# Performance work log

Measured on AMD Instinct MI355X. Metric: run time of the kernel, lower is better.

## Reference

```python
import jax, jax.numpy as jnp
import numpy as np


def _build_tree(N: int, n: int, seed: int = 0):
    """Random forest encoded as parent pointers + sibling ranks.

    parents:  int32 [N+1]; parents[i] in [0, i) for i>0, root(0) and sentinel(N) -> N.
    child_pos: int32 [N+1]; rank among siblings (in_edges order); >= n means the
               one-hot code is all zeros (matches torch.eye rows beyond n, and roots).
    """
    rng = np.random.default_rng(seed)
    parents = np.empty(N + 1, dtype=np.int32)
    parents[0] = N                      # root -> sentinel
    parents[1:N] = rng.integers(0, np.arange(1, N))  # parent of i is an earlier node
    parents[N] = N                      # sentinel self-loop

    pa = parents[:N].astype(np.int64)
    order = np.argsort(pa, kind="stable")
    sorted_pa = pa[order]
    _, first_idx, inv = np.unique(sorted_pa, return_index=True, return_inverse=True)
    rank = np.arange(N) - first_idx[inv]           # sibling rank within each parent group
    child_pos = np.empty(N + 1, dtype=np.int32)
    child_pos[order] = rank.astype(np.int32)
    child_pos[0] = n                    # root has no parent -> zero code
    child_pos[N] = n                    # sentinel -> zero code
    return parents, child_pos


def setup_inputs() -> dict:
    N, n, k = 262144, 32, 16
    parents, child_pos = _build_tree(N, n)
    return {
        "parents": jnp.asarray(parents),
        "child_pos": jnp.asarray(child_pos),
        "n": n,
        "k": k,
    }


def reference(parents, child_pos, n, k):
    """pos_embeds[node] = concat_{t=0..k-1} onehot(child_pos(ancestor_t(node)), n).

    This is the closed form of the original layer-by-layer scatter:
      pos[child, :n]  = eye row (sibling rank one-hot)
      pos[child, n:]  = pos[parent, :-n]
    Roots keep all-zero codes (child_pos = n -> out-of-range one-hot = zeros).
    """
    N = parents.shape[0] - 1

    def step(cur, _):
        code = jax.nn.one_hot(child_pos[cur], n, dtype=jnp.float32)  # [N, n]
        return parents[cur], code

    _, codes = jax.lax.scan(step, jnp.arange(N, dtype=parents.dtype), None, length=k)
    # codes: [k, N, n] -> [N, k*n] with slot 0 (own code) first
    return jnp.transpose(codes, (1, 0, 2)).reshape(N, k * n)
```

## Files before the change

kernel.cpp:

```cpp
#include <hip/hip_runtime.h>


#define NN 32
#define KK 16

typedef float f32x4 __attribute__((ext_vector_type(4)));

__global__ __launch_bounds__(256) void pe_fused_rl(
    const int* __restrict__ parents,
    const int* __restrict__ child_pos,
    f32x4* __restrict__ out4, int N)
{
    const int lane  = (int)(threadIdx.x & 63);
    const int wid   = (int)((blockIdx.x * blockDim.x + threadIdx.x) >> 6);
    const int wbase = wid * 64;
    const int node  = wbase + lane;

    unsigned int c[4];
    {
        int cur = (node < N) ? node : N;
        #pragma unroll
        for (int w = 0; w < 4; ++w) {
            unsigned int u = 0;
            #pragma unroll
            for (int b = 0; b < 4; ++b) {
                const int cp = child_pos[cur];
                const unsigned int byte = (cp < NN) ? (unsigned int)cp : 0xFFu;
                u |= byte << (8 * b);
                cur = parents[cur];
            }
            c[w] = u;
        }
    }

    const bool hi32 = (lane >= 32);
    const int  sh   = ((lane >> 3) & 3) * 8;
    const int  q4   = (lane & 7) * 4;

    f32x4* wout = out4 + (size_t)wbase * 128 + lane;

    #pragma unroll 4
    for (int r = 0; r < 64; ++r) {
        const unsigned s0 = (unsigned)__builtin_amdgcn_readlane((int)c[0], r);
        const unsigned s1 = (unsigned)__builtin_amdgcn_readlane((int)c[1], r);
        const unsigned s2 = (unsigned)__builtin_amdgcn_readlane((int)c[2], r);
        const unsigned s3 = (unsigned)__builtin_amdgcn_readlane((int)c[3], r);

        const int code0 = (int)(((hi32 ? s1 : s0) >> sh) & 0xFFu);
        const int code1 = (int)(((hi32 ? s3 : s2) >> sh) & 0xFFu);

        f32x4 v0, v1;
        v0.x = (code0 == q4    ) ? 1.0f : 0.0f;
        v0.y = (code0 == q4 + 1) ? 1.0f : 0.0f;
        v0.z = (code0 == q4 + 2) ? 1.0f : 0.0f;
        v0.w = (code0 == q4 + 3) ? 1.0f : 0.0f;
        v1.x = (code1 == q4    ) ? 1.0f : 0.0f;
        v1.y = (code1 == q4 + 1) ? 1.0f : 0.0f;
        v1.z = (code1 == q4 + 2) ? 1.0f : 0.0f;
        v1.w = (code1 == q4 + 3) ? 1.0f : 0.0f;

        __builtin_nontemporal_store(v0, &wout[(size_t)r * 128]);
        __builtin_nontemporal_store(v1, &wout[(size_t)r * 128 + 64]);
    }
}

extern "C" void kernel_launch(void* const* d_in, const int* in_sizes, int n_in,
                              void* d_out, int out_size, void* d_ws, size_t ws_size,
                              hipStream_t stream) {
    const int* parents   = (const int*)d_in[0];
    const int* child_pos = (const int*)d_in[1];
    f32x4* out4 = (f32x4*)d_out;

    const int N = in_sizes[0] - 1;
    const int n_waves = (N + 63) / 64;
    const int grid    = (n_waves + 3) / 4;

    pe_fused_rl<<<grid, 256, 0, stream>>>(parents, child_pos, out4, N);
}
```

Measured before the change: 111.7 us.

## Process four node groups per wave and switch to regular stores

Each wavefront now handles 256 nodes instead of 64, walking four independent ancestor chains at once so the dependent gather loads overlap and hide latency. The grid shrinks fourfold. Output stores change from nontemporal to ordinary stores. The cost is fewer waves in flight, which lowers occupancy on an output-bandwidth-bound kernel, plus more registers per thread.

```diff
diff --git a/kernel.cpp b/kernel.cpp
--- a/kernel.cpp
+++ b/kernel.cpp
@@ -6,61 +6,70 @@
 
 typedef float f32x4 __attribute__((ext_vector_type(4)));
 
-__global__ __launch_bounds__(256) void pe_fused_rl(
+__global__ __launch_bounds__(256) void pe_fused_lo(
     const int* __restrict__ parents,
     const int* __restrict__ child_pos,
     f32x4* __restrict__ out4, int N)
 {
     const int lane  = (int)(threadIdx.x & 63);
     const int wid   = (int)((blockIdx.x * blockDim.x + threadIdx.x) >> 6);
-    const int wbase = wid * 64;
-    const int node  = wbase + lane;
+    const int wbase = wid * 256;
 
-    unsigned int c[4];
-    {
-        int cur = (node < N) ? node : N;
+    unsigned int c[4][4];
+    int cur[4];
+    #pragma unroll
+    for (int q = 0; q < 4; ++q) {
+        int n0 = wbase + q * 64 + lane;
+        cur[q] = (n0 < N) ? n0 : N;
+    }
+    #pragma unroll
+    for (int w = 0; w < 4; ++w) {
+        unsigned int u[4] = {0, 0, 0, 0};
         #pragma unroll
-        for (int w = 0; w < 4; ++w) {
-            unsigned int u = 0;
+        for (int b = 0; b < 4; ++b) {
             #pragma unroll
-            for (int b = 0; b < 4; ++b) {
-                const int cp = child_pos[cur];
+            for (int q = 0; q < 4; ++q) {
+                const int cp = child_pos[cur[q]];
                 const unsigned int byte = (cp < NN) ? (unsigned int)cp : 0xFFu;
-                u |= byte << (8 * b);
-                cur = parents[cur];
+                u[q] |= byte << (8 * b);
+                cur[q] = parents[cur[q]];
             }
-            c[w] = u;
         }
+        #pragma unroll
+        for (int q = 0; q < 4; ++q) c[q][w] = u[q];
     }
 
     const bool hi32 = (lane >= 32);
     const int  sh   = ((lane >> 3) & 3) * 8;
     const int  q4   = (lane & 7) * 4;
 
-    f32x4* wout = out4 + (size_t)wbase * 128 + lane;
+    #pragma unroll
+    for (int q = 0; q < 4; ++q) {
+        if (wbase + q * 64 >= N) break;
+        f32x4* wout = out4 + (size_t)(wbase + q * 64) * 128 + lane;
+        #pragma unroll 4
+        for (int j = 0; j < 64; ++j) {
+            const unsigned s0 = (unsigned)__builtin_amdgcn_readlane((int)c[q][0], j);
+            const unsigned s1 = (unsigned)__builtin_amdgcn_readlane((int)c[q][1], j);
+            const unsigned s2 = (unsigned)__builtin_amdgcn_readlane((int)c[q][2], j);
+            const unsigned s3 = (unsigned)__builtin_amdgcn_readlane((int)c[q][3], j);
 
-    #pragma unroll 4
-    for (int r = 0; r < 64; ++r) {
-        const unsigned s0 = (unsigned)__builtin_amdgcn_readlane((int)c[0], r);
-        const unsigned s1 = (unsigned)__builtin_amdgcn_readlane((int)c[1], r);
-        const unsigned s2 = (unsigned)__builtin_amdgcn_readlane((int)c[2], r);
-        const unsigned s3 = (unsigned)__builtin_amdgcn_readlane((int)c[3], r);
+            const int code0 = (int)(((hi32 ? s1 : s0) >> sh) & 0xFFu);
+            const int code1 = (int)(((hi32 ? s3 : s2) >> sh) & 0xFFu);
 
-        const int code0 = (int)(((hi32 ? s1 : s0) >> sh) & 0xFFu);
-        const int code1 = (int)(((hi32 ? s3 : s2) >> sh) & 0xFFu);
+            f32x4 v0, v1;
+            v0.x = (code0 == q4    ) ? 1.0f : 0.0f;
+            v0.y = (code0 == q4 + 1) ? 1.0f : 0.0f;
+            v0.z = (code0 == q4 + 2) ? 1.0f : 0.0f;
+            v0.w = (code0 == q4 + 3) ? 1.0f : 0.0f;
+            v1.x = (code1 == q4    ) ? 1.0f : 0.0f;
+            v1.y = (code1 == q4 + 1) ? 1.0f : 0.0f;
+            v1.z = (code1 == q4 + 2) ? 1.0f : 0.0f;
+            v1.w = (code1 == q4 + 3) ? 1.0f : 0.0f;
 
-        f32x4 v0, v1;
-        v0.x = (code0 == q4    ) ? 1.0f : 0.0f;
-        v0.y = (code0 == q4 + 1) ? 1.0f : 0.0f;
-        v0.z = (code0 == q4 + 2) ? 1.0f : 0.0f;
-        v0.w = (code0 == q4 + 3) ? 1.0f : 0.0f;
-        v1.x = (code1 == q4    ) ? 1.0f : 0.0f;
-        v1.y = (code1 == q4 + 1) ? 1.0f : 0.0f;
-        v1.z = (code1 == q4 + 2) ? 1.0f : 0.0f;
-        v1.w = (code1 == q4 + 3) ? 1.0f : 0.0f;
-
-        __builtin_nontemporal_store(v0, &wout[(size_t)r * 128]);
-        __builtin_nontemporal_store(v1, &wout[(size_t)r * 128 + 64]);
+            wout[(size_t)j * 128]      = v0;
+            wout[(size_t)j * 128 + 64] = v1;
+        }
     }
 }
 
@@ -72,8 +81,8 @@
     f32x4* out4 = (f32x4*)d_out;
 
     const int N = in_sizes[0] - 1;
-    const int n_waves = (N + 63) / 64;
+    const int n_waves = (N + 255) / 256;
     const int grid    = (n_waves + 3) / 4;
 
-    pe_fused_rl<<<grid, 256, 0, stream>>>(parents, child_pos, out4, N);
+    pe_fused_lo<<<grid, 256, 0, stream>>>(parents, child_pos, out4, N);
 }
```

Measured after the change: 111.9 us. About the same (+0.2%).
